# Optimization experiments

Hardware: AMD Instinct MI355X
Metric: run time of the kernel (lower is better)

The kernel has to match this reference:

```python
import jax, jax.numpy as jnp
import numpy as np

T = 25_000_000   # total jagged values across all keys
F = 8            # number of feature keys
L = 200          # max feature length (position table size per key)
BAG = 50         # fixed bag length used to synthesize realistic positions


def setup_inputs() -> dict:
    key = jax.random.key(0)
    k_pw, = jax.random.split(key, 1)
    # learned per-key position weight tables (module inits to 1.0; randn for testing)
    position_weights = jax.random.normal(k_pw, (F, L), dtype=jnp.float32)
    # per-key contiguous key ids (torch.split over length_per_key => sorted blocks)
    key_ids = jnp.repeat(jnp.arange(F, dtype=jnp.int32), T // F)
    # offsets_range pattern: position-within-bag, here bags of fixed length BAG
    positions = jnp.tile(jnp.arange(BAG, dtype=jnp.int32), T // BAG)
    return {"position_weights": position_weights, "key_ids": key_ids, "positions": positions}


def reference(position_weights, key_ids, positions):
    # Fused equivalent of: split by length_per_key, per-key
    # torch.gather(position_weights[key], 0, pos), then cat.
    # weight[t] = position_weights[key_ids[t], positions[t]]
    return position_weights[key_ids, positions]
```

## Files before the change

kernel.cpp:

```cpp
#include <hip/hip_runtime.h>

#define NKEYS 8
#define MAXLEN 200
#define TBL_SZ (NKEYS * MAXLEN)
#define BLOCK 256

__global__ __launch_bounds__(BLOCK) void pw_gather_kernel(
    const float* __restrict__ pw,
    const int*   __restrict__ keys,
    const int*   __restrict__ poss,
    float*       __restrict__ out,
    int n)
{
    __shared__ float tbl[TBL_SZ];
    for (int i = threadIdx.x; i < TBL_SZ; i += BLOCK) {
        tbl[i] = pw[i];
    }
    __syncthreads();

    int idx = blockIdx.x * BLOCK + threadIdx.x;
    long base = (long)idx * 4;
    if (base + 3 < n) {
        int4 k = ((const int4*)keys)[idx];
        int4 p = ((const int4*)poss)[idx];
        float4 o;
        o.x = tbl[k.x * MAXLEN + p.x];
        o.y = tbl[k.y * MAXLEN + p.y];
        o.z = tbl[k.z * MAXLEN + p.z];
        o.w = tbl[k.w * MAXLEN + p.w];
        ((float4*)out)[idx] = o;
    } else {
        for (long j = base; j < n; ++j) {
            out[j] = tbl[keys[j] * MAXLEN + poss[j]];
        }
    }
}

extern "C" void kernel_launch(void* const* d_in, const int* in_sizes, int n_in,
                              void* d_out, int out_size, void* d_ws, size_t ws_size,
                              hipStream_t stream) {
    const float* pw   = (const float*)d_in[0];
    const int*   keys = (const int*)d_in[1];
    const int*   poss = (const int*)d_in[2];
    float*       out  = (float*)d_out;

    int n  = in_sizes[1];
    int n4 = (n + 3) / 4;
    int blocks = (n4 + BLOCK - 1) / BLOCK;

    pw_gather_kernel<<<blocks, BLOCK, 0, stream>>>(pw, keys, poss, out, n);
}
```

Before: 242.7 us.

## Use persistent grid-stride loop with software-prefetched index loads

Caps the grid at 2048 blocks and has each thread walk a grid-stride loop, so the shared-memory table fill is paid once per persistent block instead of once per 256x4 elements. The next iteration's key and position vectors are loaded before the current gather and store, to overlap global loads with LDS lookups. The cost is fewer resident waves to hide memory latency and a tail handled serially by one thread.

```diff
diff --git a/kernel.cpp b/kernel.cpp
--- a/kernel.cpp
+++ b/kernel.cpp
@@ -4,6 +4,10 @@
 #define MAXLEN 200
 #define TBL_SZ (NKEYS * MAXLEN)
 #define BLOCK 256
+#define GRID 2048
+
+typedef float f32x4 __attribute__((ext_vector_type(4)));
+typedef int   i32x4 __attribute__((ext_vector_type(4)));
 
 __global__ __launch_bounds__(BLOCK) void pw_gather_kernel(
     const float* __restrict__ pw,
@@ -18,19 +22,41 @@
     }
     __syncthreads();
 
+    const int n4     = n >> 2;
+    const int stride = gridDim.x * BLOCK;
+
     int idx = blockIdx.x * BLOCK + threadIdx.x;
-    long base = (long)idx * 4;
-    if (base + 3 < n) {
-        int4 k = ((const int4*)keys)[idx];
-        int4 p = ((const int4*)poss)[idx];
-        float4 o;
+
+    i32x4 k, p;
+    bool have = idx < n4;
+    if (have) {
+        k = ((const i32x4*)keys)[idx];
+        p = ((const i32x4*)poss)[idx];
+    }
+    while (have) {
+        const int  nidx  = idx + stride;
+        const bool hnext = nidx < n4;
+        i32x4 kn, pn;
+        if (hnext) {
+            kn = ((const i32x4*)keys)[nidx];
+            pn = ((const i32x4*)poss)[nidx];
+        }
+
+        f32x4 o;
         o.x = tbl[k.x * MAXLEN + p.x];
         o.y = tbl[k.y * MAXLEN + p.y];
         o.z = tbl[k.z * MAXLEN + p.z];
         o.w = tbl[k.w * MAXLEN + p.w];
-        ((float4*)out)[idx] = o;
-    } else {
-        for (long j = base; j < n; ++j) {
+        ((f32x4*)out)[idx] = o;
+
+        idx  = nidx;
+        k    = kn;
+        p    = pn;
+        have = hnext;
+    }
+
+    if (blockIdx.x == 0 && threadIdx.x == 0) {
+        for (int j = n4 * 4; j < n; ++j) {
             out[j] = tbl[keys[j] * MAXLEN + poss[j]];
         }
     }
@@ -46,7 +72,8 @@
 
     int n  = in_sizes[1];
     int n4 = (n + 3) / 4;
-    int blocks = (n4 + BLOCK - 1) / BLOCK;
+    int blocks_needed = (n4 + BLOCK - 1) / BLOCK;
+    int blocks = blocks_needed < GRID ? blocks_needed : GRID;
 
     pw_gather_kernel<<<blocks, BLOCK, 0, stream>>>(pw, keys, poss, out, n);
 }
```

New measurement: 249.1 us. 1.03x slower.
